# Performance work log

Measured on AMD Instinct MI355X. Metric: run time of the kernel, lower is better.

The kernel has to match this reference:

```python
import jax, jax.numpy as jnp
import numpy as np

EMBED_DIM = 1024
NUM_HEADS = 16
HEAD_DIM = EMBED_DIM // NUM_HEADS


def setup_inputs() -> dict:
    key = jax.random.key(0)
    ks = jax.random.split(key, 5)
    B, N, C = 4, 2048, EMBED_DIM
    x = jax.random.normal(ks[0], (B, N, C), dtype=jnp.float32)
    # Linear params (PyTorch layout: weight [out, in])
    s = 1.0 / np.sqrt(C)
    W_qkv = jax.random.uniform(ks[1], (3 * C, C), dtype=jnp.float32, minval=-s, maxval=s)
    b_qkv = jax.random.uniform(ks[2], (3 * C,), dtype=jnp.float32, minval=-s, maxval=s)
    W_out = jax.random.uniform(ks[3], (C, C), dtype=jnp.float32, minval=-s, maxval=s)
    b_out = jax.random.uniform(ks[4], (C,), dtype=jnp.float32, minval=-s, maxval=s)
    return {"x": x, "W_qkv": W_qkv, "b_qkv": b_qkv, "W_out": W_out, "b_out": b_out}


def _rotate_half(t):
    t1, t2 = jnp.split(t, 2, axis=-1)
    return jnp.concatenate((-t2, t1), axis=-1)


def _rope_cos_sin(seq_len, dim, dtype):
    inv_freq = 1.0 / (10000.0 ** (jnp.arange(0, dim, 2, dtype=jnp.float32) / dim))
    t = jnp.arange(seq_len, dtype=jnp.float32)
    freqs = jnp.einsum("i,j->ij", t, inv_freq)  # [N, dim/2]
    emb = jnp.concatenate((freqs, freqs), axis=-1)  # [N, dim]
    return emb.astype(dtype)


def reference(x, W_qkv, b_qkv, W_out, b_out):
    B, N, C = x.shape
    H, D = NUM_HEADS, HEAD_DIM
    qkv = x @ W_qkv.T + b_qkv  # [B, N, 3C]
    qkv = qkv.reshape(B, N, 3, H, D).transpose(2, 0, 3, 1, 4)  # [3, B, H, N, D]
    q, k, v = qkv[0], qkv[1], qkv[2]
    emb = _rope_cos_sin(N, D, x.dtype)
    cos = jnp.cos(emb)[None, None, :, :]  # [1,1,N,D]
    sin = jnp.sin(emb)[None, None, :, :]
    q = q * cos + _rotate_half(q) * sin
    k = k * cos + _rotate_half(k) * sin
    scale = D ** -0.5
    attn = jnp.einsum("bhnd,bhmd->bhnm", q, k) * scale  # [B,H,N,N]
    attn = jax.nn.softmax(attn, axis=-1)
    out = jnp.einsum("bhnm,bhmd->bhnd", attn, v)  # [B,H,N,D]
    out = out.transpose(0, 2, 1, 3).reshape(B, N, C)
    return out @ W_out.T + b_out
```

## Files before the change

### kernel.cpp

```cpp
#include <hip/hip_runtime.h>
#include <hip/hip_bf16.h>
#include <cstdint>
#include <cstddef>

#define SEQ 2048
#define NBATCH 4
#define EMB 1024
#define NH 16
#define HD 64
#define MTOT (NBATCH * SEQ)

typedef __attribute__((ext_vector_type(8))) short bf16x8;
typedef __attribute__((ext_vector_type(4))) float f32x4;
typedef __attribute__((ext_vector_type(16))) float f32x16;
typedef unsigned short u16;
typedef unsigned int u32;

__device__ __forceinline__ float bf2f(u16 v) {
  union { u32 u; float f; } c; c.u = ((u32)v) << 16; return c.f;
}
__device__ __forceinline__ u16 f2bf(float f) {
  union { float f; u32 u; } c; c.f = f;
  u32 u = c.u;
  return (u16)((u + 0x7FFFu + ((u >> 16) & 1u)) >> 16);
}
__device__ __forceinline__ u32 f2u(float f) {
  union { float f; u32 u; } c; c.f = f; return c.u;
}

__global__ void prep_kernel(const float* __restrict__ x, const float* __restrict__ wqkv,
                            const float* __restrict__ wout,
                            u16* __restrict__ xb, u16* __restrict__ wqkvb,
                            u16* __restrict__ woutb, float* __restrict__ tab2) {
  int tid = blockIdx.x * blockDim.x + threadIdx.x;
  int stride = gridDim.x * blockDim.x;
  for (int i = tid; i < MTOT * EMB / 4; i += stride) {
    float4 v = reinterpret_cast<const float4*>(x)[i];
    ushort4 o;
    o.x = f2bf(v.x); o.y = f2bf(v.y); o.z = f2bf(v.z); o.w = f2bf(v.w);
    reinterpret_cast<ushort4*>(xb)[i] = o;
  }
  for (int i = tid; i < 3 * EMB * EMB / 4; i += stride) {
    float4 v = reinterpret_cast<const float4*>(wqkv)[i];
    ushort4 o;
    o.x = f2bf(v.x); o.y = f2bf(v.y); o.z = f2bf(v.z); o.w = f2bf(v.w);
    reinterpret_cast<ushort4*>(wqkvb)[i] = o;
  }
  for (int i = tid; i < EMB * EMB / 4; i += stride) {
    float4 v = reinterpret_cast<const float4*>(wout)[i];
    ushort4 o;
    o.x = f2bf(v.x); o.y = f2bf(v.y); o.z = f2bf(v.z); o.w = f2bf(v.w);
    reinterpret_cast<ushort4*>(woutb)[i] = o;
  }
  for (int i = tid; i < SEQ * 32; i += stride) {
    int n = i >> 5, j = i & 31;
    float invf = 1.0f / powf(10000.0f, (float)(2 * j) / 64.0f);
    float ang = (float)n * invf;
    tab2[2 * i] = cosf(ang);
    tab2[2 * i + 1] = sinf(ang);
  }
}

__device__ __forceinline__ void gld_lds16(const u16* g, u16* l) {
  __builtin_amdgcn_global_load_lds((const __attribute__((address_space(1))) void*)g,
                                   (__attribute__((address_space(3))) void*)l, 16, 0, 0);
}

__global__ __launch_bounds__(256, 2)
void gemm_bt_f32(const u16* __restrict__ A, const u16* __restrict__ Bw,
                 const float* __restrict__ bias, float* __restrict__ Cout,
                 int N, int tiles_n) {
  __shared__ u16 lA[128 * 64];
  __shared__ u16 lB[128 * 64];
  const int K = 1024;
  int g = blockIdx.x;
  int xcd = g & 7, idx = g >> 3;
  int bm = (idx & 7) * 8 + xcd;
  int bn = idx >> 3;
  int t = threadIdx.x;
  int wave = t >> 6, lane = t & 63;
  int wm = wave >> 1, wn = wave & 1;
  int l15 = lane & 15, l4 = lane >> 4;

  f32x4 acc[4][4];
#pragma unroll
  for (int i = 0; i < 4; ++i)
#pragma unroll
    for (int j = 0; j < 4; ++j) acc[i][j] = (f32x4){0.f, 0.f, 0.f, 0.f};

  int su[4], sr[4], sc[4];
#pragma unroll
  for (int i = 0; i < 4; ++i) {
    int u = (i * 4 + wave) * 64 + lane;
    su[i] = u;
    sr[i] = u >> 3;
    sc[i] = (u & 7) ^ (sr[i] & 7);
  }

  for (int kt = 0; kt < K / 64; ++kt) {
    if (kt) __syncthreads();
#pragma unroll
    for (int i = 0; i < 4; ++i) {
      gld_lds16(A + (size_t)(bm * 128 + sr[i]) * K + kt * 64 + sc[i] * 8, &lA[su[i] * 8]);
      gld_lds16(Bw + (size_t)(bn * 128 + sr[i]) * K + kt * 64 + sc[i] * 8, &lB[su[i] * 8]);
    }
    __syncthreads();
#pragma unroll
    for (int ks = 0; ks < 2; ++ks) {
      bf16x8 af[4], bfr[4];
#pragma unroll
      for (int mb = 0; mb < 4; ++mb) {
        int r = wm * 64 + mb * 16 + l15;
        int cc = (ks * 4 + l4) ^ (r & 7);
        af[mb] = *reinterpret_cast<const bf16x8*>(&lA[r * 64 + cc * 8]);
      }
#pragma unroll
      for (int nb = 0; nb < 4; ++nb) {
        int r = wn * 64 + nb * 16 + l15;
        int cc = (ks * 4 + l4) ^ (r & 7);
        bfr[nb] = *reinterpret_cast<const bf16x8*>(&lB[r * 64 + cc * 8]);
      }
#pragma unroll
      for (int mb = 0; mb < 4; ++mb)
#pragma unroll
        for (int nb = 0; nb < 4; ++nb)
          acc[mb][nb] = __builtin_amdgcn_mfma_f32_16x16x32_bf16(af[mb], bfr[nb], acc[mb][nb], 0, 0, 0);
    }
  }

#pragma unroll
  for (int mb = 0; mb < 4; ++mb)
#pragma unroll
    for (int nb = 0; nb < 4; ++nb) {
      int row0 = bm * 128 + wm * 64 + mb * 16 + l4 * 4;
      int col = bn * 128 + wn * 64 + nb * 16 + l15;
      float bv = bias[col];
#pragma unroll
      for (int r = 0; r < 4; ++r)
        Cout[(size_t)(row0 + r) * N + col] = acc[mb][nb][r] + bv;
    }
}

__global__ __launch_bounds__(256, 2)
void gemm_qkv_rope(const u16* __restrict__ A, const u16* __restrict__ Bw,
                   const float* __restrict__ bias, const float* __restrict__ tab2,
                   u16* __restrict__ Qb, u16* __restrict__ Kb, u16* __restrict__ Vtb) {
  __shared__ u16 lA[128 * 64];
  __shared__ u16 lB[128 * 64];
  const int K = 1024;
  int g = blockIdx.x;
  int xcd = g & 7, idx = g >> 3;
  int bm = (idx & 7) * 8 + xcd;
  int bn = idx >> 3;
  int t = threadIdx.x;
  int wave = t >> 6, lane = t & 63;
  int wm = wave >> 1, wn = wave & 1;
  int l15 = lane & 15, l4 = lane >> 4;

  f32x4 acc[4][4];
#pragma unroll
  for (int i = 0; i < 4; ++i)
#pragma unroll
    for (int j = 0; j < 4; ++j) acc[i][j] = (f32x4){0.f, 0.f, 0.f, 0.f};

  int su[4], sr[4], sc[4];
#pragma unroll
  for (int i = 0; i < 4; ++i) {
    int u = (i * 4 + wave) * 64 + lane;
    su[i] = u;
    sr[i] = u >> 3;
    sc[i] = (u & 7) ^ (sr[i] & 7);
  }
  int tauB[4];
#pragma unroll
  for (int i = 0; i < 4; ++i) {
    int rr = sr[i] & 63;
    tauB[i] = (sr[i] & 64) | (rr & 32) | ((rr & 15) << 1) | ((rr >> 4) & 1);
  }

  for (int kt = 0; kt < K / 64; ++kt) {
    if (kt) __syncthreads();
#pragma unroll
    for (int i = 0; i < 4; ++i) {
      gld_lds16(A + (size_t)(bm * 128 + sr[i]) * K + kt * 64 + sc[i] * 8, &lA[su[i] * 8]);
      gld_lds16(Bw + (size_t)(bn * 128 + tauB[i]) * K + kt * 64 + sc[i] * 8, &lB[su[i] * 8]);
    }
    __syncthreads();
#pragma unroll
    for (int ks = 0; ks < 2; ++ks) {
      bf16x8 af[4], bfr[4];
#pragma unroll
      for (int mb = 0; mb < 4; ++mb) {
        int r = wm * 64 + mb * 16 + l15;
        int cc = (ks * 4 + l4) ^ (r & 7);
        af[mb] = *reinterpret_cast<const bf16x8*>(&lA[r * 64 + cc * 8]);
      }
#pragma unroll
      for (int nb = 0; nb < 4; ++nb) {
        int r = wn * 64 + nb * 16 + l15;
        int cc = (ks * 4 + l4) ^ (r & 7);
        bfr[nb] = *reinterpret_cast<const bf16x8*>(&lB[r * 64 + cc * 8]);
      }
#pragma unroll
      for (int mb = 0; mb < 4; ++mb)
#pragma unroll
        for (int nb = 0; nb < 4; ++nb)
          acc[mb][nb] = __builtin_amdgcn_mfma_f32_16x16x32_bf16(af[mb], bfr[nb], acc[mb][nb], 0, 0, 0);
    }
  }

  int type = bn >> 3;
  int h = (bn * 2 + wn) & 15;
  int colbase = bn * 128 + wn * 64;
  float bv[4];
#pragma unroll
  for (int nb = 0; nb < 4; ++nb)
    bv[nb] = bias[colbase + 32 * (nb >> 1) + 2 * l15 + (nb & 1)];

  if (type < 2) {
    u16* dst0 = (type == 0) ? Qb : Kb;
    float qs = (type == 0) ? 0.1803368801111163f : 1.0f;
#pragma unroll
    for (int mb = 0; mb < 4; ++mb) {
      int row0 = bm * 128 + wm * 64 + mb * 16 + l4 * 4;
#pragma unroll
      for (int r = 0; r < 4; ++r) {
        int row = row0 + r;
        int bb = row >> 11, nl = row & 2047;
        float4 cs4 = *reinterpret_cast<const float4*>(tab2 + (size_t)nl * 64 + 4 * l15);
        float a0 = acc[mb][0][r] + bv[0];
        float a1 = acc[mb][1][r] + bv[1];
        float a2 = acc[mb][2][r] + bv[2];
        float a3 = acc[mb][3][r] + bv[3];
        float o0 = (a0 * cs4.x - a2 * cs4.y) * qs;
        float o2 = (a2 * cs4.x + a0 * cs4.y) * qs;
        float o1 = (a1 * cs4.z - a3 * cs4.w) * qs;
        float o3 = (a3 * cs4.z + a1 * cs4.w) * qs;
        u16* dst = dst0 + ((size_t)(bb * 16 + h) * SEQ + nl) * 64;
        u32 lo = (u32)f2bf(o0) | ((u32)f2bf(o1) << 16);
        u32 hi2 = (u32)f2bf(o2) | ((u32)f2bf(o3) << 16);
        *reinterpret_cast<u32*>(&dst[2 * l15]) = lo;
        *reinterpret_cast<u32*>(&dst[32 + 2 * l15]) = hi2;
      }
    }
  } else {
#pragma unroll
    for (int mb = 0; mb < 4; ++mb) {
      int row0 = bm * 128 + wm * 64 + mb * 16 + l4 * 4;
      int bb = row0 >> 11, nl0 = row0 & 2047;
#pragma unroll
      for (int nb = 0; nb < 4; ++nb) {
        int d = 32 * (nb >> 1) + 2 * l15 + (nb & 1);
        ushort4 pk;
        pk.x = f2bf(acc[mb][nb][0] + bv[nb]);
        pk.y = f2bf(acc[mb][nb][1] + bv[nb]);
        pk.z = f2bf(acc[mb][nb][2] + bv[nb]);
        pk.w = f2bf(acc[mb][nb][3] + bv[nb]);
        *reinterpret_cast<ushort4*>(&Vtb[((size_t)(bb * 16 + h) * 64 + d) * SEQ + nl0]) = pk;
      }
    }
  }
}

__global__ __launch_bounds__(256, 4)
void attn_kernel(const u16* __restrict__ Q, const u16* __restrict__ Kk,
                 const u16* __restrict__ Vt, u16* __restrict__ Out) {
  int bid = blockIdx.x;
  int swz = (bid & 7) * 128 + (bid >> 3);
  int bh = swz >> 4;
  int qt = swz & 15;
  int b = bh >> 4, h = bh & 15;
  int t = threadIdx.x;
  int wave = t >> 6, lane = t & 63;
  int l31 = lane & 31, hi = lane >> 5;

  __shared__ u16 lK[2][520 * 8];
  __shared__ u16 lV[2][520 * 8];

  const u16* Qh = Q + (size_t)bh * SEQ * 64;
  const u16* Kh = Kk + (size_t)bh * SEQ * 64;
  const u16* Vh = Vt + (size_t)bh * 64 * SEQ;
  int q0w = qt * 128 + wave * 32;

  bf16x8 qf[4];
#pragma unroll
  for (int dc = 0; dc < 4; ++dc)
    qf[dc] = *reinterpret_cast<const bf16x8*>(
        &Qh[(size_t)(q0w + l31) * 64 + dc * 16 + hi * 8]);

  f32x16 oacc[2];
#pragma unroll
  for (int db = 0; db < 2; ++db)
#pragma unroll
    for (int r = 0; r < 16; ++r) oacc[db][r] = 0.f;
  float dn = 0.f;

  bf16x8 kreg[2], vreg[2];
  auto stage_load = [&](int kt) {
#pragma unroll
    for (int p = 0; p < 2; ++p) {
      int u = p * 256 + t;
      int r = u >> 3, c = u & 7;
      kreg[p] = *reinterpret_cast<const bf16x8*>(&Kh[(size_t)(kt * 64 + r) * 64 + c * 8]);
      vreg[p] = *reinterpret_cast<const bf16x8*>(&Vh[(size_t)r * SEQ + kt * 64 + c * 8]);
    }
  };
  auto stage_write = [&](int buf) {
#pragma unroll
    for (int p = 0; p < 2; ++p) {
      int u = p * 256 + t;
      int r = u >> 3, c = u & 7;
      *reinterpret_cast<bf16x8*>(&lK[buf][(c * 65 + r) * 8]) = kreg[p];
      *reinterpret_cast<bf16x8*>(&lV[buf][(c * 65 + r) * 8]) = vreg[p];
    }
  };

  union PF { u32 w[4]; bf16x8 v; };
  int cur = 0;
  stage_load(0);
  stage_write(0);
  __syncthreads();
  for (int kt = 0; kt < SEQ / 64; ++kt) {
    if (kt + 1 < SEQ / 64) stage_load(kt + 1);

    f32x16 s[2];
#pragma unroll
    for (int cb = 0; cb < 2; ++cb)
#pragma unroll
      for (int r = 0; r < 16; ++r) s[cb][r] = 0.f;
    __builtin_amdgcn_s_setprio(1);
#pragma unroll
    for (int cb = 0; cb < 2; ++cb) {
#pragma unroll
      for (int dc = 0; dc < 4; ++dc) {
        bf16x8 kf = *reinterpret_cast<const bf16x8*>(
            &lK[cur][((dc * 2 + hi) * 65 + cb * 32 + l31) * 8]);
        s[cb] = __builtin_amdgcn_mfma_f32_32x32x16_bf16(kf, qf[dc], s[cb], 0, 0, 0);
      }
    }
    __builtin_amdgcn_s_setprio(0);

    PF pa[2][2];
#pragma unroll
    for (int cb = 0; cb < 2; ++cb) {
#pragma unroll
      for (int r = 0; r < 16; ++r) {
        float e = __builtin_amdgcn_exp2f(s[cb][r]);
        s[cb][r] = e;
        dn += e;
      }
#pragma unroll
      for (int c = 0; c < 2; ++c) {
        u32 u0 = f2u(s[cb][8 * c + 0]) + 0x8000u;
        u32 u1 = f2u(s[cb][8 * c + 1]) + 0x8000u;
        u32 u2 = f2u(s[cb][8 * c + 2]) + 0x8000u;
        u32 u3 = f2u(s[cb][8 * c + 3]) + 0x8000u;
        u32 u4 = f2u(s[cb][8 * c + 4]) + 0x8000u;
        u32 u5 = f2u(s[cb][8 * c + 5]) + 0x8000u;
        u32 u6 = f2u(s[cb][8 * c + 6]) + 0x8000u;
        u32 u7 = f2u(s[cb][8 * c + 7]) + 0x8000u;
        u32 a1 = __builtin_amdgcn_perm(u1, u0, 0x07060302);
        u32 a2 = __builtin_amdgcn_perm(u3, u2, 0x07060302);
        u32 b1 = __builtin_amdgcn_perm(u5, u4, 0x07060302);
        u32 b2 = __builtin_amdgcn_perm(u7, u6, 0x07060302);
        asm("v_permlane32_swap_b32 %0, %1" : "+v"(a1), "+v"(b1));
        asm("v_permlane32_swap_b32 %0, %1" : "+v"(a2), "+v"(b2));
        pa[cb][c].w[0] = a1; pa[cb][c].w[1] = a2;
        pa[cb][c].w[2] = b1; pa[cb][c].w[3] = b2;
      }
    }

    __builtin_amdgcn_s_setprio(1);
#pragma unroll
    for (int cb = 0; cb < 2; ++cb)
#pragma unroll
      for (int c = 0; c < 2; ++c)
#pragma unroll
        for (int db = 0; db < 2; ++db) {
          bf16x8 vf = *reinterpret_cast<const bf16x8*>(
              &lV[cur][((cb * 4 + c * 2 + hi) * 65 + db * 32 + l31) * 8]);
          oacc[db] = __builtin_amdgcn_mfma_f32_32x32x16_bf16(pa[cb][c].v, vf, oacc[db], 0, 0, 0);
        }
    __builtin_amdgcn_s_setprio(0);

    if (kt + 1 < SEQ / 64) stage_write(cur ^ 1);
    __syncthreads();
    cur ^= 1;
  }

  dn += __shfl_xor(dn, 32);
#pragma unroll
  for (int r = 0; r < 16; ++r) {
    int qrel = (r & 3) + 8 * (r >> 2) + 4 * hi;
    float dfull = __shfl(dn, qrel);
    float inv = __builtin_amdgcn_rcpf(dfull);
    int q = q0w + qrel;
#pragma unroll
    for (int db = 0; db < 2; ++db) {
      int d = db * 32 + l31;
      Out[(size_t)(b * SEQ + q) * EMB + h * 64 + d] = f2bf(oacc[db][r] * inv);
    }
  }
}

extern "C" void kernel_launch(void* const* d_in, const int* in_sizes, int n_in,
                              void* d_out, int out_size, void* d_ws, size_t ws_size,
                              hipStream_t stream) {
  const float* x = (const float*)d_in[0];
  const float* bqkv = (const float*)d_in[2];
  const float* bout = (const float*)d_in[4];
  float* out = (float*)d_out;

  char* ws = (char*)d_ws;
  size_t off = 0;
  auto alloc = [&](size_t bytes) {
    void* p = ws + off;
    off += (bytes + 255) & ~(size_t)255;
    return p;
  };
  u16* xb    = (u16*)alloc((size_t)MTOT * EMB * 2);
  u16* wqkvb = (u16*)alloc((size_t)3 * EMB * EMB * 2);
  u16* woutb = (u16*)alloc((size_t)EMB * EMB * 2);
  u16* Qb    = (u16*)alloc((size_t)64 * SEQ * HD * 2);
  u16* Kb    = (u16*)alloc((size_t)64 * SEQ * HD * 2);
  u16* Vtb   = (u16*)alloc((size_t)64 * HD * SEQ * 2);
  u16* aout  = (u16*)alloc((size_t)MTOT * EMB * 2);
  float* tab2 = (float*)alloc((size_t)SEQ * 32 * 2 * 4);
  (void)ws_size; (void)in_sizes; (void)n_in; (void)out_size;

  prep_kernel<<<4096, 256, 0, stream>>>(x, (const float*)d_in[1], (const float*)d_in[3],
                                        xb, wqkvb, woutb, tab2);
  gemm_qkv_rope<<<64 * 24, 256, 0, stream>>>(xb, wqkvb, bqkv, tab2, Qb, Kb, Vtb);
  attn_kernel<<<64 * 16, 256, 0, stream>>>(Qb, Kb, Vtb, aout);
  gemm_bt_f32<<<64 * 8, 256, 0, stream>>>(aout, woutb, bout, out, EMB, 8);
}
```

Baseline: 176.2 us.

## Process two query blocks per wave in attention to reuse K/V fragments

Each wave now computes 64 query rows (two 32-row MFMA blocks) instead of 32, sharing every K and V LDS fragment load across both blocks. The grid is halved and the block swizzle adjusted, and launch bounds are relaxed to allow more registers per thread. This is meant to cut LDS and global K/V traffic per unit of MFMA work. The cost is higher register pressure and fewer resident waves to hide latency.

```diff
diff --git a/kernel.cpp b/kernel.cpp
--- a/kernel.cpp
+++ b/kernel.cpp
@@ -262,13 +262,13 @@
   }
 }
 
-__global__ __launch_bounds__(256, 4)
+__global__ __launch_bounds__(256, 2)
 void attn_kernel(const u16* __restrict__ Q, const u16* __restrict__ Kk,
                  const u16* __restrict__ Vt, u16* __restrict__ Out) {
   int bid = blockIdx.x;
-  int swz = (bid & 7) * 128 + (bid >> 3);
-  int bh = swz >> 4;
-  int qt = swz & 15;
+  int swz = (bid & 7) * 64 + (bid >> 3);
+  int bh = swz >> 3;
+  int qt = swz & 7;
   int b = bh >> 4, h = bh & 15;
   int t = threadIdx.x;
   int wave = t >> 6, lane = t & 63;
@@ -280,20 +280,27 @@
   const u16* Qh = Q + (size_t)bh * SEQ * 64;
   const u16* Kh = Kk + (size_t)bh * SEQ * 64;
   const u16* Vh = Vt + (size_t)bh * 64 * SEQ;
-  int q0w = qt * 128 + wave * 32;
-
-  bf16x8 qf[4];
-#pragma unroll
-  for (int dc = 0; dc < 4; ++dc)
-    qf[dc] = *reinterpret_cast<const bf16x8*>(
-        &Qh[(size_t)(q0w + l31) * 64 + dc * 16 + hi * 8]);
-
-  f32x16 oacc[2];
-#pragma unroll
-  for (int db = 0; db < 2; ++db)
-#pragma unroll
-    for (int r = 0; r < 16; ++r) oacc[db][r] = 0.f;
-  float dn = 0.f;
+  int q0w = qt * 256 + wave * 64;
+
+  bf16x8 qf[2][4];
+#pragma unroll
+  for (int qb = 0; qb < 2; ++qb)
+#pragma unroll
+    for (int dc = 0; dc < 4; ++dc)
+      qf[qb][dc] = *reinterpret_cast<const bf16x8*>(
+          &Qh[(size_t)(q0w + qb * 32 + l31) * 64 + dc * 16 + hi * 8]);
+
+  f32x16 oacc[2][2];
+#pragma unroll
+  for (int qb = 0; qb < 2; ++qb)
+#pragma unroll
+    for (int db = 0; db < 2; ++db)
+#pragma unroll
+      for (int r = 0; r < 16; ++r) oacc[qb][db][r] = 0.f;
+  f32x16 zacc;
+#pragma unroll
+  for (int r = 0; r < 16; ++r) zacc[r] = 0.f;
+  float dn[2] = {0.f, 0.f};
 
   bf16x8 kreg[2], vreg[2];
   auto stage_load = [&](int kt) {
@@ -323,11 +330,7 @@
   for (int kt = 0; kt < SEQ / 64; ++kt) {
     if (kt + 1 < SEQ / 64) stage_load(kt + 1);
 
-    f32x16 s[2];
-#pragma unroll
-    for (int cb = 0; cb < 2; ++cb)
-#pragma unroll
-      for (int r = 0; r < 16; ++r) s[cb][r] = 0.f;
+    f32x16 s[2][2];
     __builtin_amdgcn_s_setprio(1);
 #pragma unroll
     for (int cb = 0; cb < 2; ++cb) {
@@ -335,40 +338,43 @@
       for (int dc = 0; dc < 4; ++dc) {
         bf16x8 kf = *reinterpret_cast<const bf16x8*>(
             &lK[cur][((dc * 2 + hi) * 65 + cb * 32 + l31) * 8]);
-        s[cb] = __builtin_amdgcn_mfma_f32_32x32x16_bf16(kf, qf[dc], s[cb], 0, 0, 0);
+        s[0][cb] = __builtin_amdgcn_mfma_f32_32x32x16_bf16(kf, qf[0][dc], dc ? s[0][cb] : zacc, 0, 0, 0);
+        s[1][cb] = __builtin_amdgcn_mfma_f32_32x32x16_bf16(kf, qf[1][dc], dc ? s[1][cb] : zacc, 0, 0, 0);
       }
     }
     __builtin_amdgcn_s_setprio(0);
 
-    PF pa[2][2];
-#pragma unroll
-    for (int cb = 0; cb < 2; ++cb) {
-#pragma unroll
-      for (int r = 0; r < 16; ++r) {
-        float e = __builtin_amdgcn_exp2f(s[cb][r]);
-        s[cb][r] = e;
-        dn += e;
-      }
-#pragma unroll
-      for (int c = 0; c < 2; ++c) {
-        u32 u0 = f2u(s[cb][8 * c + 0]) + 0x8000u;
-        u32 u1 = f2u(s[cb][8 * c + 1]) + 0x8000u;
-        u32 u2 = f2u(s[cb][8 * c + 2]) + 0x8000u;
-        u32 u3 = f2u(s[cb][8 * c + 3]) + 0x8000u;
-        u32 u4 = f2u(s[cb][8 * c + 4]) + 0x8000u;
-        u32 u5 = f2u(s[cb][8 * c + 5]) + 0x8000u;
-        u32 u6 = f2u(s[cb][8 * c + 6]) + 0x8000u;
-        u32 u7 = f2u(s[cb][8 * c + 7]) + 0x8000u;
-        u32 a1 = __builtin_amdgcn_perm(u1, u0, 0x07060302);
-        u32 a2 = __builtin_amdgcn_perm(u3, u2, 0x07060302);
-        u32 b1 = __builtin_amdgcn_perm(u5, u4, 0x07060302);
-        u32 b2 = __builtin_amdgcn_perm(u7, u6, 0x07060302);
-        asm("v_permlane32_swap_b32 %0, %1" : "+v"(a1), "+v"(b1));
-        asm("v_permlane32_swap_b32 %0, %1" : "+v"(a2), "+v"(b2));
-        pa[cb][c].w[0] = a1; pa[cb][c].w[1] = a2;
-        pa[cb][c].w[2] = b1; pa[cb][c].w[3] = b2;
-      }
-    }
+    PF pa[2][2][2];
+#pragma unroll
+    for (int qb = 0; qb < 2; ++qb)
+#pragma unroll
+      for (int cb = 0; cb < 2; ++cb) {
+#pragma unroll
+        for (int r = 0; r < 16; ++r) {
+          float e = __builtin_amdgcn_exp2f(s[qb][cb][r]);
+          s[qb][cb][r] = e;
+          dn[qb] += e;
+        }
+#pragma unroll
+        for (int c = 0; c < 2; ++c) {
+          u32 u0 = f2u(s[qb][cb][8 * c + 0]) + 0x8000u;
+          u32 u1 = f2u(s[qb][cb][8 * c + 1]) + 0x8000u;
+          u32 u2 = f2u(s[qb][cb][8 * c + 2]) + 0x8000u;
+          u32 u3 = f2u(s[qb][cb][8 * c + 3]) + 0x8000u;
+          u32 u4 = f2u(s[qb][cb][8 * c + 4]) + 0x8000u;
+          u32 u5 = f2u(s[qb][cb][8 * c + 5]) + 0x8000u;
+          u32 u6 = f2u(s[qb][cb][8 * c + 6]) + 0x8000u;
+          u32 u7 = f2u(s[qb][cb][8 * c + 7]) + 0x8000u;
+          u32 a1 = __builtin_amdgcn_perm(u1, u0, 0x07060302);
+          u32 a2 = __builtin_amdgcn_perm(u3, u2, 0x07060302);
+          u32 b1 = __builtin_amdgcn_perm(u5, u4, 0x07060302);
+          u32 b2 = __builtin_amdgcn_perm(u7, u6, 0x07060302);
+          asm("v_permlane32_swap_b32 %0, %1" : "+v"(a1), "+v"(b1));
+          asm("v_permlane32_swap_b32 %0, %1" : "+v"(a2), "+v"(b2));
+          pa[qb][cb][c].w[0] = a1; pa[qb][cb][c].w[1] = a2;
+          pa[qb][cb][c].w[2] = b1; pa[qb][cb][c].w[3] = b2;
+        }
+      }
 
     __builtin_amdgcn_s_setprio(1);
 #pragma unroll
@@ -379,7 +385,8 @@
         for (int db = 0; db < 2; ++db) {
           bf16x8 vf = *reinterpret_cast<const bf16x8*>(
               &lV[cur][((cb * 4 + c * 2 + hi) * 65 + db * 32 + l31) * 8]);
-          oacc[db] = __builtin_amdgcn_mfma_f32_32x32x16_bf16(pa[cb][c].v, vf, oacc[db], 0, 0, 0);
+          oacc[0][db] = __builtin_amdgcn_mfma_f32_32x32x16_bf16(pa[0][cb][c].v, vf, oacc[0][db], 0, 0, 0);
+          oacc[1][db] = __builtin_amdgcn_mfma_f32_32x32x16_bf16(pa[1][cb][c].v, vf, oacc[1][db], 0, 0, 0);
         }
     __builtin_amdgcn_s_setprio(0);
 
@@ -388,19 +395,22 @@
     cur ^= 1;
   }
 
-  dn += __shfl_xor(dn, 32);
-#pragma unroll
-  for (int r = 0; r < 16; ++r) {
-    int qrel = (r & 3) + 8 * (r >> 2) + 4 * hi;
-    float dfull = __shfl(dn, qrel);
-    float inv = __builtin_amdgcn_rcpf(dfull);
-    int q = q0w + qrel;
-#pragma unroll
-    for (int db = 0; db < 2; ++db) {
-      int d = db * 32 + l31;
-      Out[(size_t)(b * SEQ + q) * EMB + h * 64 + d] = f2bf(oacc[db][r] * inv);
-    }
-  }
+#pragma unroll
+  for (int qb = 0; qb < 2; ++qb) dn[qb] += __shfl_xor(dn[qb], 32);
+#pragma unroll
+  for (int qb = 0; qb < 2; ++qb)
+#pragma unroll
+    for (int r = 0; r < 16; ++r) {
+      int qrel = (r & 3) + 8 * (r >> 2) + 4 * hi;
+      float dfull = __shfl(dn[qb], qrel);
+      float inv = __builtin_amdgcn_rcpf(dfull);
+      int q = q0w + qb * 32 + qrel;
+#pragma unroll
+      for (int db = 0; db < 2; ++db) {
+        int d = db * 32 + l31;
+        Out[(size_t)(b * SEQ + q) * EMB + h * 64 + d] = f2bf(oacc[qb][db][r] * inv);
+      }
+    }
 }
 
 extern "C" void kernel_launch(void* const* d_in, const int* in_sizes, int n_in,
@@ -431,6 +441,6 @@
   prep_kernel<<<4096, 256, 0, stream>>>(x, (const float*)d_in[1], (const float*)d_in[3],
                                         xb, wqkvb, woutb, tab2);
   gemm_qkv_rope<<<64 * 24, 256, 0, stream>>>(xb, wqkvb, bqkv, tab2, Qb, Kb, Vtb);
-  attn_kernel<<<64 * 16, 256, 0, stream>>>(Qb, Kb, Vtb, aout);
+  attn_kernel<<<64 * 8, 256, 0, stream>>>(Qb, Kb, Vtb, aout);
   gemm_bt_f32<<<64 * 8, 256, 0, stream>>>(aout, woutb, bout, out, EMB, 8);
 }
```

New measurement: 171.0 us. 1.03x faster.
